# Optimization experiments

Measured on AMD Instinct MI355X. Metric: run time of the kernel, lower is better.

Reference implementation:

```python
import jax, jax.numpy as jnp
import numpy as np

NUM_CENTROID = 64
HIDDEN = 768
MAX_SEQ = 128
D = MAX_SEQ * HIDDEN  # 98304 flattened feature dim
NUM_ITERS = 10        # fixed Lloyd iterations (original loops to tol; fixed for jit)


def _cdist(x, c):
    x2 = jnp.sum(x * x, axis=-1, keepdims=True)          # [N,1]
    c2 = jnp.sum(c * c, axis=-1)                          # [K]
    d2 = x2 + c2[None, :] - 2.0 * (x @ c.T)               # [N,K]
    return jnp.sqrt(jnp.maximum(d2, 0.0))


def setup_inputs() -> dict:
    key = jax.random.key(0)
    k1, k2 = jax.random.split(key)
    x = jax.random.normal(k1, (1024, MAX_SEQ, HIDDEN), dtype=jnp.float32)
    # centroid table initialized as Normal(mean=0.07, std=0.39) per the module
    centroid = 0.07 + 0.39 * jax.random.normal(k2, (NUM_CENTROID, D), dtype=jnp.float32)
    return {"x": x, "centroid": centroid}


def reference(x, centroid):
    X = x.reshape(-1, D)                                  # [N, D]
    N = X.shape[0]
    # 'resuming' branch: snap each centroid to its nearest sample
    dis0 = _cdist(X, centroid)                            # [N, K]
    choice_points = jnp.argmin(dis0, axis=0)              # [K]
    state = X[choice_points]                              # [K, D]
    ones = jnp.ones((N,), dtype=X.dtype)

    def step(state, _):
        dis = _cdist(X, state)                            # [N, K]
        choice = jnp.argmin(dis, axis=1)                  # [N]
        sums = jax.ops.segment_sum(X, choice, num_segments=NUM_CENTROID)   # [K, D]
        counts = jax.ops.segment_sum(ones, choice, num_segments=NUM_CENTROID)  # [K]
        nonempty = counts[:, None] > 0
        new_state = jnp.where(nonempty, sums / jnp.maximum(counts[:, None], 1.0), state)
        return new_state, choice

    state, choices = jax.lax.scan(step, state, None, length=NUM_ITERS)
    # returns (new centroids, final cluster assignments) like the module
    return state, choices[-1]
```

## Files before the change

### kernel.cpp

```cpp
#include <hip/hip_runtime.h>
#include <cstddef>
#include <cstdint>


#define N_PTS  1024
#define K_C    64
#define D_DIM  98304
#define ITERS  10
#define SPLITD 64
#define BM     64
#define DC     64
#define LDSP   72
#define NCHK   96
#define CCHK   12

typedef __attribute__((ext_vector_type(8))) short bf16x8;
typedef __attribute__((ext_vector_type(8))) unsigned short ushort8;
typedef __attribute__((ext_vector_type(4))) float f32x4;

__device__ __forceinline__ unsigned short f2bf(float x) {
    unsigned u = __float_as_uint(x);
    u = (u + 0x7FFFu + ((u >> 16) & 1u)) >> 16;
    return (unsigned short)u;
}
__device__ __forceinline__ float bf2f(unsigned short b) {
    return __uint_as_float((unsigned)b << 16);
}
__device__ __forceinline__ void cvt2(float x, unsigned short& h, unsigned short& l) {
    h = f2bf(x);
    l = f2bf(x - bf2f(h));
}

__device__ __forceinline__ float block_sum256(float s) {
    #pragma unroll
    for (int o = 32; o; o >>= 1) s += __shfl_down(s, o);
    __shared__ float red[4];
    int lane = threadIdx.x & 63, w = threadIdx.x >> 6;
    if (lane == 0) red[w] = s;
    __syncthreads();
    return red[0] + red[1] + red[2] + red[3];
}

__global__ __launch_bounds__(256) void convert_kernel(const float* __restrict__ A,
                                                      unsigned short* __restrict__ Ph,
                                                      unsigned short* __restrict__ Pl,
                                                      float* __restrict__ sq_part) {
    const int n = blockIdx.x, j = blockIdx.y;
    const size_t base = (size_t)n * D_DIM + (size_t)j * 8192;
    const int t = threadIdx.x;
    float ss = 0.f;
    #pragma unroll
    for (int i = 0; i < 4; ++i) {
        size_t e = base + (size_t)i * 2048 + t * 8;
        float4 a = *reinterpret_cast<const float4*>(A + e);
        float4 b = *reinterpret_cast<const float4*>(A + e + 4);
        ss += a.x*a.x + a.y*a.y + a.z*a.z + a.w*a.w;
        ss += b.x*b.x + b.y*b.y + b.z*b.z + b.w*b.w;
        ushort4 h0, l0, h1, l1;
        cvt2(a.x, h0.x, l0.x); cvt2(a.y, h0.y, l0.y);
        cvt2(a.z, h0.z, l0.z); cvt2(a.w, h0.w, l0.w);
        cvt2(b.x, h1.x, l1.x); cvt2(b.y, h1.y, l1.y);
        cvt2(b.z, h1.z, l1.z); cvt2(b.w, h1.w, l1.w);
        *reinterpret_cast<ushort4*>(Ph + e)     = h0;
        *reinterpret_cast<ushort4*>(Ph + e + 4) = h1;
        *reinterpret_cast<ushort4*>(Pl + e)     = l0;
        *reinterpret_cast<ushort4*>(Pl + e + 4) = l1;
    }
    ss = block_sum256(ss);
    if (t == 0) sq_part[n * CCHK + j] = ss;
}

__global__ __launch_bounds__(256) void reduce_sq_kernel(const float* __restrict__ sq_part,
                                                        float* __restrict__ out, int rows) {
    int n = blockIdx.x * 256 + threadIdx.x;
    if (n >= rows) return;
    float s = 0.f;
    #pragma unroll
    for (int j = 0; j < CCHK; ++j) s += sq_part[n * CCHK + j];
    out[n] = s;
}

__global__ __launch_bounds__(256, 5) void mfma_dot_kernel(const unsigned short* __restrict__ Xh,
                                                          const unsigned short* __restrict__ Xl,
                                                          const unsigned short* __restrict__ Sh,
                                                          const unsigned short* __restrict__ Sl,
                                                          float* __restrict__ partial) {
    __shared__ alignas(16) short Bh[K_C][LDSP];
    __shared__ alignas(16) short Bl[K_C][LDSP];

    const int seg = blockIdx.x, nblk = blockIdx.y;
    const int t = threadIdx.x;
    const int wid = t >> 6, lane = t & 63;
    const int d_begin = seg * (D_DIM / SPLITD);
    const int NCH = (D_DIM / SPLITD) / DC;

    const int arow = nblk * BM + wid * 16 + (lane & 15);
    const int ko = (lane >> 4) * 8;
    const unsigned short* xh = Xh + (size_t)arow * D_DIM;
    const unsigned short* xl = Xl + (size_t)arow * D_DIM;

    const int sr = t >> 2, sc = (t & 3) * 16;
    const unsigned short* shp = Sh + (size_t)sr * D_DIM;
    const unsigned short* slp = Sl + (size_t)sr * D_DIM;

    ushort8 s0, s1, s2, s3;
    bf16x8 aEh0, aEh1, aEl0, aEl1;
    bf16x8 aOh0, aOh1, aOl0, aOl1;

    auto loadB = [&](int d0) {
        s0 = *reinterpret_cast<const ushort8*>(shp + d0 + sc);
        s1 = *reinterpret_cast<const ushort8*>(shp + d0 + sc + 8);
        s2 = *reinterpret_cast<const ushort8*>(slp + d0 + sc);
        s3 = *reinterpret_cast<const ushort8*>(slp + d0 + sc + 8);
    };
    auto storeB = [&]() {
        *reinterpret_cast<ushort8*>(&Bh[sr][sc])     = s0;
        *reinterpret_cast<ushort8*>(&Bh[sr][sc + 8]) = s1;
        *reinterpret_cast<ushort8*>(&Bl[sr][sc])     = s2;
        *reinterpret_cast<ushort8*>(&Bl[sr][sc + 8]) = s3;
    };

    f32x4 acc[4];
    #pragma unroll
    for (int i = 0; i < 4; ++i) acc[i] = f32x4{0.f, 0.f, 0.f, 0.f};

    #define LOADA(bh0, bh1, bl0, bl1, d0)                                        \
        bh0 = *reinterpret_cast<const bf16x8*>(xh + (d0) + ko);                  \
        bh1 = *reinterpret_cast<const bf16x8*>(xh + (d0) + 32 + ko);             \
        bl0 = *reinterpret_cast<const bf16x8*>(xl + (d0) + ko);                  \
        bl1 = *reinterpret_cast<const bf16x8*>(xl + (d0) + 32 + ko);

    #define MFMAS(ah0, ah1, al0, al1)                                            \
        _Pragma("unroll")                                                        \
        for (int nb = 0; nb < 4; ++nb) {                                         \
            const int br = nb * 16 + (lane & 15);                                \
            bf16x8 bh = *reinterpret_cast<const bf16x8*>(&Bh[br][ko]);           \
            bf16x8 bl = *reinterpret_cast<const bf16x8*>(&Bl[br][ko]);           \
            acc[nb] = __builtin_amdgcn_mfma_f32_16x16x32_bf16(ah0, bh, acc[nb], 0, 0, 0); \
            acc[nb] = __builtin_amdgcn_mfma_f32_16x16x32_bf16(ah0, bl, acc[nb], 0, 0, 0); \
            acc[nb] = __builtin_amdgcn_mfma_f32_16x16x32_bf16(al0, bh, acc[nb], 0, 0, 0); \
        }                                                                        \
        _Pragma("unroll")                                                        \
        for (int nb = 0; nb < 4; ++nb) {                                         \
            const int br = nb * 16 + (lane & 15);                                \
            bf16x8 bh = *reinterpret_cast<const bf16x8*>(&Bh[br][32 + ko]);      \
            bf16x8 bl = *reinterpret_cast<const bf16x8*>(&Bl[br][32 + ko]);      \
            acc[nb] = __builtin_amdgcn_mfma_f32_16x16x32_bf16(ah1, bh, acc[nb], 0, 0, 0); \
            acc[nb] = __builtin_amdgcn_mfma_f32_16x16x32_bf16(ah1, bl, acc[nb], 0, 0, 0); \
            acc[nb] = __builtin_amdgcn_mfma_f32_16x16x32_bf16(al1, bh, acc[nb], 0, 0, 0); \
        }

    loadB(d_begin);
    LOADA(aEh0, aEh1, aEl0, aEl1, d_begin);
    for (int c = 0; c < NCH; c += 2) {
        __syncthreads();
        storeB();
        __syncthreads();
        {
            int dn = d_begin + (c + 1) * DC;
            loadB(dn);
            LOADA(aOh0, aOh1, aOl0, aOl1, dn);
        }
        MFMAS(aEh0, aEh1, aEl0, aEl1);
        __syncthreads();
        storeB();
        __syncthreads();
        if (c + 2 < NCH) {
            int dn = d_begin + (c + 2) * DC;
            loadB(dn);
            LOADA(aEh0, aEh1, aEl0, aEl1, dn);
        }
        MFMAS(aOh0, aOh1, aOl0, aOl1);
    }
    #undef LOADA
    #undef MFMAS

    #pragma unroll
    for (int nb = 0; nb < 4; ++nb)
        #pragma unroll
        for (int r = 0; r < 4; ++r) {
            int row = wid * 16 + (lane >> 4) * 4 + r;
            int col = nb * 16 + (lane & 15);
            int n = nblk * BM + row;
            partial[((size_t)seg * N_PTS + n) * K_C + col] = acc[nb][r];
        }
}

__global__ __launch_bounds__(256) void reduce_dot_kernel(const float* __restrict__ partial,
                                                         float* __restrict__ dot) {
    int i = blockIdx.x * 256 + threadIdx.x;
    float s = 0.f;
    #pragma unroll 8
    for (int p = 0; p < SPLITD; ++p) s += partial[(size_t)p * N_PTS * K_C + i];
    dot[i] = s;
}

__global__ __launch_bounds__(256) void argmin_n_kernel(const float* __restrict__ dot,
                                                       const float* __restrict__ x2,
                                                       int* __restrict__ choice_pts) {
    int k = blockIdx.x;
    float best = 3.4e38f; int bi = N_PTS;
    for (int n = threadIdx.x; n < N_PTS; n += 256) {
        float v = fmaf(-2.f, dot[n * K_C + k], x2[n]);
        if (v < best || (v == best && n < bi)) { best = v; bi = n; }
    }
    #pragma unroll
    for (int off = 32; off; off >>= 1) {
        float v2 = __shfl_down(best, off);
        int   i2 = __shfl_down(bi, off);
        if (v2 < best || (v2 == best && i2 < bi)) { best = v2; bi = i2; }
    }
    __shared__ float bv[4]; __shared__ int bix[4];
    int lane = threadIdx.x & 63, wid = threadIdx.x >> 6;
    if (lane == 0) { bv[wid] = best; bix[wid] = bi; }
    __syncthreads();
    if (threadIdx.x == 0) {
        for (int w = 1; w < 4; ++w)
            if (bv[w] < best || (bv[w] == best && bix[w] < bi)) { best = bv[w]; bi = bix[w]; }
        choice_pts[k] = bi;
    }
}

__global__ __launch_bounds__(256) void gather_kernel(const float* __restrict__ X,
                                                     const int* __restrict__ choice_pts,
                                                     float* __restrict__ state,
                                                     unsigned short* __restrict__ Sh,
                                                     unsigned short* __restrict__ Sl,
                                                     float* __restrict__ c2p) {
    int k = blockIdx.x;
    int c = choice_pts[k];
    size_t d = (size_t)blockIdx.y * 1024 + threadIdx.x * 4;
    size_t o = (size_t)k * D_DIM + d;
    float4 v = *reinterpret_cast<const float4*>(X + (size_t)c * D_DIM + d);
    *reinterpret_cast<float4*>(state + o) = v;
    ushort4 h, l;
    cvt2(v.x, h.x, l.x); cvt2(v.y, h.y, l.y); cvt2(v.z, h.z, l.z); cvt2(v.w, h.w, l.w);
    *reinterpret_cast<ushort4*>(Sh + o) = h;
    *reinterpret_cast<ushort4*>(Sl + o) = l;
    float ss = block_sum256(v.x*v.x + v.y*v.y + v.z*v.z + v.w*v.w);
    if (threadIdx.x == 0) c2p[k * NCHK + blockIdx.y] = ss;
}

__global__ __launch_bounds__(256) void assign_kernel(const float* __restrict__ partial,
                                                     const float* __restrict__ c2p,
                                                     int* __restrict__ choice) {
    int wid = threadIdx.x >> 6, lane = threadIdx.x & 63;
    int n = blockIdx.x * 4 + wid;
    float s = 0.f;
    #pragma unroll 8
    for (int p = 0; p < SPLITD; ++p) s += partial[((size_t)p * N_PTS + n) * K_C + lane];
    float c2 = 0.f;
    const float* cp2 = c2p + lane * NCHK;
    #pragma unroll 8
    for (int j = 0; j < NCHK; ++j) c2 += cp2[j];
    float v = fmaf(-2.f, s, c2);
    int bi = lane;
    #pragma unroll
    for (int m = 32; m; m >>= 1) {
        float v2 = __shfl_xor(v, m);
        int   i2 = __shfl_xor(bi, m);
        if (v2 < v || (v2 == v && i2 < bi)) { v = v2; bi = i2; }
    }
    if (lane == 0) choice[n] = bi;
}

__global__ __launch_bounds__(256) void init_prev_kernel(int* __restrict__ chp,
                                                        int* __restrict__ ctp) {
    int t = blockIdx.x * 256 + threadIdx.x;
    if (t < N_PTS) chp[t] = -1;
    if (t < K_C)   ctp[t] = 0;
}

__global__ __launch_bounds__(1024) void changes_kernel(const int* __restrict__ ch_new,
                                                       const int* __restrict__ ch_prev,
                                                       int* __restrict__ add_n,
                                                       int* __restrict__ astart,
                                                       int* __restrict__ sub_n,
                                                       int* __restrict__ sstart,
                                                       int* __restrict__ counts_new) {
    __shared__ int chn[N_PTS];
    __shared__ int chp[N_PTS];
    __shared__ int acnt[K_C], scnt[K_C], hcnt[K_C];
    __shared__ int ast[K_C + 1], sst[K_C + 1];
    const int t = threadIdx.x;
    if (t < K_C) { acnt[t] = 0; scnt[t] = 0; hcnt[t] = 0; }
    __syncthreads();
    const int cn = ch_new[t], cp = ch_prev[t];
    chn[t] = cn; chp[t] = cp;
    atomicAdd(&hcnt[cn], 1);
    const bool changed = (cn != cp);
    if (changed) {
        atomicAdd(&acnt[cn], 1);
        if (cp >= 0) atomicAdd(&scnt[cp], 1);
    }
    __syncthreads();
    if (t == 0) {
        int a = 0;
        for (int k = 0; k < K_C; ++k) { ast[k] = a; a += acnt[k]; }
        ast[K_C] = a;
    }
    if (t == 64) {
        int a = 0;
        for (int k = 0; k < K_C; ++k) { sst[k] = a; a += scnt[k]; }
        sst[K_C] = a;
    }
    __syncthreads();
    int ra = 0, rs = 0;
    for (int m = 0; m < t; ++m) {
        int cm = chn[m], pm = chp[m];
        bool ch = (cm != pm);
        ra += (ch && cm == cn);
        rs += (ch && pm == cp);
    }
    if (changed) {
        add_n[ast[cn] + ra] = t;
        if (cp >= 0) sub_n[sst[cp] + rs] = t;
    }
    if (t <= K_C) { astart[t] = ast[t]; sstart[t] = sst[t]; }
    if (t < K_C) counts_new[t] = hcnt[t];
}

__global__ __launch_bounds__(256) void update_kernel(const float* __restrict__ X,
                                                     const int* __restrict__ add_n,
                                                     const int* __restrict__ astart,
                                                     const int* __restrict__ sub_n,
                                                     const int* __restrict__ sstart,
                                                     const int* __restrict__ counts_new,
                                                     const int* __restrict__ counts_prev,
                                                     float* __restrict__ state,
                                                     unsigned short* __restrict__ Sh,
                                                     unsigned short* __restrict__ Sl,
                                                     float* __restrict__ c2p) {
    const int k = blockIdx.x;
    const int ab = astart[k], ae = astart[k + 1];
    const int sb = sstart[k], se = sstart[k + 1];
    if (ab == ae && sb == se) return;
    const int cn = counts_new[k], cp = counts_prev[k];
    const size_t d = (size_t)blockIdx.y * 1024 + threadIdx.x * 4;
    const size_t o = (size_t)k * D_DIM + d;

    float sx = 0.f, sy = 0.f, sz = 0.f, sw = 0.f;
    if (cp > 0) {
        float4 st = *reinterpret_cast<const float4*>(state + o);
        float c = (float)cp;
        sx = st.x * c; sy = st.y * c; sz = st.z * c; sw = st.w * c;
    }
    for (int i = ab; i < ae; ++i) {
        const float4 v = *reinterpret_cast<const float4*>(X + (size_t)add_n[i] * D_DIM + d);
        sx += v.x; sy += v.y; sz += v.z; sw += v.w;
    }
    for (int i = sb; i < se; ++i) {
        const float4 v = *reinterpret_cast<const float4*>(X + (size_t)sub_n[i] * D_DIM + d);
        sx -= v.x; sy -= v.y; sz -= v.z; sw -= v.w;
    }
    if (cn > 0) {
        float inv = 1.f / (float)cn;
        float4 m; m.x = sx * inv; m.y = sy * inv; m.z = sz * inv; m.w = sw * inv;
        *reinterpret_cast<float4*>(state + o) = m;
        ushort4 h, l;
        cvt2(m.x, h.x, l.x); cvt2(m.y, h.y, l.y); cvt2(m.z, h.z, l.z); cvt2(m.w, h.w, l.w);
        *reinterpret_cast<ushort4*>(Sh + o) = h;
        *reinterpret_cast<ushort4*>(Sl + o) = l;
        float ss = block_sum256(m.x*m.x + m.y*m.y + m.z*m.z + m.w*m.w);
        if (threadIdx.x == 0) c2p[k * NCHK + blockIdx.y] = ss;
    }
}

__global__ __launch_bounds__(256) void choice_out_kernel(const int* __restrict__ choice,
                                                         float* __restrict__ out) {
    int n = blockIdx.x * 256 + threadIdx.x;
    if (n < N_PTS) out[n] = (float)choice[n];
}

extern "C" void kernel_launch(void* const* d_in, const int* in_sizes, int n_in,
                              void* d_out, int out_size, void* d_ws, size_t ws_size,
                              hipStream_t stream) {
    const float* X  = (const float*)d_in[0];
    const float* C0 = (const float*)d_in[1];
    float* state      = (float*)d_out;
    float* out_choice = state + (size_t)K_C * D_DIM;

    char* w = (char*)d_ws;
    size_t off = 0;
    auto alloc = [&](size_t bytes) { void* p = w + off; off = (off + bytes + 255) & ~(size_t)255; return p; };
    unsigned short* Xh = (unsigned short*)alloc((size_t)N_PTS * D_DIM * 2);
    unsigned short* Xl = (unsigned short*)alloc((size_t)N_PTS * D_DIM * 2);
    unsigned short* Sh = (unsigned short*)alloc((size_t)K_C * D_DIM * 2);
    unsigned short* Sl = (unsigned short*)alloc((size_t)K_C * D_DIM * 2);
    float* partial = (float*)alloc((size_t)SPLITD * N_PTS * K_C * 4);
    float* dotb    = (float*)alloc((size_t)N_PTS * K_C * 4);
    float* x2p     = (float*)alloc((size_t)N_PTS * CCHK * 4);
    float* x2      = (float*)alloc((size_t)N_PTS * 4);
    float* c0sq    = (float*)alloc((size_t)K_C * CCHK * 4);
    float* c2p     = (float*)alloc((size_t)K_C * NCHK * 4);
    int* cpts      = (int*)alloc(256);
    int* ch[2];
    ch[0] = (int*)alloc((size_t)N_PTS * 4);
    ch[1] = (int*)alloc((size_t)N_PTS * 4);
    int* ct[2];
    ct[0] = (int*)alloc(256);
    ct[1] = (int*)alloc(256);
    int* add_n  = (int*)alloc((size_t)N_PTS * 4);
    int* astart = (int*)alloc(512);
    int* sub_n  = (int*)alloc((size_t)N_PTS * 4);
    int* sstart = (int*)alloc(512);

    dim3 b256(256);

    convert_kernel<<<dim3(N_PTS, CCHK), b256, 0, stream>>>(X, Xh, Xl, x2p);
    reduce_sq_kernel<<<dim3(4), b256, 0, stream>>>(x2p, x2, N_PTS);

    convert_kernel<<<dim3(K_C, CCHK), b256, 0, stream>>>(C0, Sh, Sl, c0sq);
    mfma_dot_kernel<<<dim3(SPLITD, N_PTS / BM), b256, 0, stream>>>(Xh, Xl, Sh, Sl, partial);
    reduce_dot_kernel<<<dim3(N_PTS * K_C / 256), b256, 0, stream>>>(partial, dotb);
    argmin_n_kernel<<<K_C, b256, 0, stream>>>(dotb, x2, cpts);
    gather_kernel<<<dim3(K_C, NCHK), b256, 0, stream>>>(X, cpts, state, Sh, Sl, c2p);
    init_prev_kernel<<<dim3(4), b256, 0, stream>>>(ch[0], ct[0]);

    for (int it = 0; it < ITERS; ++it) {
        int prev = it & 1, cur = 1 - prev;
        mfma_dot_kernel<<<dim3(SPLITD, N_PTS / BM), b256, 0, stream>>>(Xh, Xl, Sh, Sl, partial);
        assign_kernel<<<dim3(N_PTS / 4), b256, 0, stream>>>(partial, c2p, ch[cur]);
        changes_kernel<<<1, dim3(1024), 0, stream>>>(ch[cur], ch[prev], add_n, astart,
                                                     sub_n, sstart, ct[cur]);
        update_kernel<<<dim3(K_C, NCHK), b256, 0, stream>>>(X, add_n, astart, sub_n, sstart,
                                                            ct[cur], ct[prev], state, Sh, Sl, c2p);
    }

    choice_out_kernel<<<dim3(N_PTS / 256), b256, 0, stream>>>(ch[0], out_choice);
}
```

Baseline: 2.011 ms.

## Run Lloyd iterations in Gram-matrix space instead of recomputing full-D distances

Builds the 1024x1024 Gram matrix X·Xᵀ once with split-bf16 MFMA, then expresses every centroid dot product and centroid norm as averages of Gram entries over cluster members. Each iteration touches only the Gram matrix and small index arrays rather than the 98304-wide data. The centroid table is materialised from X only once at the end, using the last iteration in which each cluster was non-empty. This adds a large Gram build and a workspace buffer, and it changes floating-point summation order, which could flip near-tie assignments.

Result: slower. 2.179 ms (+8.4%).

```diff
diff --git a/kernel.cpp b/kernel.cpp
--- a/kernel.cpp
+++ b/kernel.cpp
@@ -13,6 +13,11 @@
 #define LDSP   72
 #define NCHK   96
 #define CCHK   12
+#define GSEG   16
+#define NPAIR  36
+#define GT     128
+#define GDC    32
+#define GLP    40
 
 typedef __attribute__((ext_vector_type(8))) short bf16x8;
 typedef __attribute__((ext_vector_type(8))) unsigned short ushort8;
@@ -223,37 +228,152 @@
 
 __global__ __launch_bounds__(256) void gather_kernel(const float* __restrict__ X,
                                                      const int* __restrict__ choice_pts,
-                                                     float* __restrict__ state,
-                                                     unsigned short* __restrict__ Sh,
-                                                     unsigned short* __restrict__ Sl,
-                                                     float* __restrict__ c2p) {
+                                                     float* __restrict__ state) {
     int k = blockIdx.x;
     int c = choice_pts[k];
     size_t d = (size_t)blockIdx.y * 1024 + threadIdx.x * 4;
-    size_t o = (size_t)k * D_DIM + d;
     float4 v = *reinterpret_cast<const float4*>(X + (size_t)c * D_DIM + d);
-    *reinterpret_cast<float4*>(state + o) = v;
-    ushort4 h, l;
-    cvt2(v.x, h.x, l.x); cvt2(v.y, h.y, l.y); cvt2(v.z, h.z, l.z); cvt2(v.w, h.w, l.w);
-    *reinterpret_cast<ushort4*>(Sh + o) = h;
-    *reinterpret_cast<ushort4*>(Sl + o) = l;
-    float ss = block_sum256(v.x*v.x + v.y*v.y + v.z*v.z + v.w*v.w);
-    if (threadIdx.x == 0) c2p[k * NCHK + blockIdx.y] = ss;
-}
-
-__global__ __launch_bounds__(256) void assign_kernel(const float* __restrict__ partial,
-                                                     const float* __restrict__ c2p,
-                                                     int* __restrict__ choice) {
+    *reinterpret_cast<float4*>(state + (size_t)k * D_DIM + d) = v;
+}
+
+__global__ __launch_bounds__(256) void gbuild_kernel(const unsigned short* __restrict__ Xh,
+                                                     const unsigned short* __restrict__ Xl,
+                                                     float* __restrict__ Gpart) {
+    __shared__ alignas(16) short Ah[GT][GLP];
+    __shared__ alignas(16) short Al[GT][GLP];
+    __shared__ alignas(16) short Bh[GT][GLP];
+    __shared__ alignas(16) short Bl[GT][GLP];
+
+    const int p = blockIdx.x, seg = blockIdx.y;
+    int bi = 0, rem = p, rl = 8;
+    while (rem >= rl) { rem -= rl; --rl; ++bi; }
+    const int bj = bi + rem;
+
+    const int t = threadIdx.x;
+    const int wid = t >> 6, lane = t & 63;
+    const int wr = wid >> 1, wc = wid & 1;
+    const int d_begin = seg * (D_DIM / GSEG);
+    const int NCH = (D_DIM / GSEG) / GDC;
+
+    const int srow = t >> 1;
+    const int scol = (t & 1) << 4;
+    const unsigned short* gah = Xh + (size_t)(bi * GT + srow) * D_DIM;
+    const unsigned short* gal = Xl + (size_t)(bi * GT + srow) * D_DIM;
+    const unsigned short* gbh = Xh + (size_t)(bj * GT + srow) * D_DIM;
+    const unsigned short* gbl = Xl + (size_t)(bj * GT + srow) * D_DIM;
+
+    ushort8 ra0, ra1, ra2, ra3, rb0, rb1, rb2, rb3;
+    auto loadRegs = [&](int d0) {
+        ra0 = *reinterpret_cast<const ushort8*>(gah + d0 + scol);
+        ra1 = *reinterpret_cast<const ushort8*>(gah + d0 + scol + 8);
+        ra2 = *reinterpret_cast<const ushort8*>(gal + d0 + scol);
+        ra3 = *reinterpret_cast<const ushort8*>(gal + d0 + scol + 8);
+        rb0 = *reinterpret_cast<const ushort8*>(gbh + d0 + scol);
+        rb1 = *reinterpret_cast<const ushort8*>(gbh + d0 + scol + 8);
+        rb2 = *reinterpret_cast<const ushort8*>(gbl + d0 + scol);
+        rb3 = *reinterpret_cast<const ushort8*>(gbl + d0 + scol + 8);
+    };
+    auto storeRegs = [&]() {
+        *reinterpret_cast<ushort8*>(&Ah[srow][scol])     = ra0;
+        *reinterpret_cast<ushort8*>(&Ah[srow][scol + 8]) = ra1;
+        *reinterpret_cast<ushort8*>(&Al[srow][scol])     = ra2;
+        *reinterpret_cast<ushort8*>(&Al[srow][scol + 8]) = ra3;
+        *reinterpret_cast<ushort8*>(&Bh[srow][scol])     = rb0;
+        *reinterpret_cast<ushort8*>(&Bh[srow][scol + 8]) = rb1;
+        *reinterpret_cast<ushort8*>(&Bl[srow][scol])     = rb2;
+        *reinterpret_cast<ushort8*>(&Bl[srow][scol + 8]) = rb3;
+    };
+
+    f32x4 acc[4][4];
+    #pragma unroll
+    for (int i = 0; i < 4; ++i)
+        #pragma unroll
+        for (int j = 0; j < 4; ++j) acc[i][j] = f32x4{0.f, 0.f, 0.f, 0.f};
+
+    const int rbase = wr * 64 + (lane & 15);
+    const int cbase = wc * 64 + (lane & 15);
+    const int ko = (lane >> 4) * 8;
+
+    loadRegs(d_begin);
+    for (int c = 0; c < NCH; ++c) {
+        __syncthreads();
+        storeRegs();
+        __syncthreads();
+        if (c + 1 < NCH) loadRegs(d_begin + (c + 1) * GDC);
+        bf16x8 fah[4], fal[4], fbh[4], fbl[4];
+        #pragma unroll
+        for (int f = 0; f < 4; ++f) {
+            fah[f] = *reinterpret_cast<const bf16x8*>(&Ah[rbase + f * 16][ko]);
+            fal[f] = *reinterpret_cast<const bf16x8*>(&Al[rbase + f * 16][ko]);
+            fbh[f] = *reinterpret_cast<const bf16x8*>(&Bh[cbase + f * 16][ko]);
+            fbl[f] = *reinterpret_cast<const bf16x8*>(&Bl[cbase + f * 16][ko]);
+        }
+        #pragma unroll
+        for (int fi = 0; fi < 4; ++fi)
+            #pragma unroll
+            for (int fj = 0; fj < 4; ++fj) {
+                acc[fi][fj] = __builtin_amdgcn_mfma_f32_16x16x32_bf16(fah[fi], fbh[fj], acc[fi][fj], 0, 0, 0);
+                acc[fi][fj] = __builtin_amdgcn_mfma_f32_16x16x32_bf16(fah[fi], fbl[fj], acc[fi][fj], 0, 0, 0);
+                acc[fi][fj] = __builtin_amdgcn_mfma_f32_16x16x32_bf16(fal[fi], fbh[fj], acc[fi][fj], 0, 0, 0);
+            }
+    }
+
+    float* gp = Gpart + ((size_t)seg * NPAIR + p) * (GT * GT);
+    #pragma unroll
+    for (int fi = 0; fi < 4; ++fi)
+        #pragma unroll
+        for (int fj = 0; fj < 4; ++fj)
+            #pragma unroll
+            for (int r = 0; r < 4; ++r) {
+                int row = wr * 64 + fi * 16 + (lane >> 4) * 4 + r;
+                int col = wc * 64 + fj * 16 + (lane & 15);
+                gp[row * GT + col] = acc[fi][fj][r];
+            }
+}
+
+__global__ __launch_bounds__(256) void reduce_g_kernel(const float* __restrict__ Gpart,
+                                                       float* __restrict__ G) {
+    const int p = blockIdx.x, blk = blockIdx.y;
+    int bi = 0, rem = p, rl = 8;
+    while (rem >= rl) { rem -= rl; --rl; ++bi; }
+    const int bj = bi + rem;
+    const int e0 = blk * 1024 + threadIdx.x * 4;
+    float sx = 0.f, sy = 0.f, sz = 0.f, sw = 0.f;
+    #pragma unroll
+    for (int g = 0; g < GSEG; ++g) {
+        const float4 v = *reinterpret_cast<const float4*>(
+            Gpart + ((size_t)g * NPAIR + p) * (GT * GT) + e0);
+        sx += v.x; sy += v.y; sz += v.z; sw += v.w;
+    }
+    const int row = e0 >> 7, col = e0 & 127;
+    const int gi = bi * GT + row, gj = bj * GT + col;
+    float4 o = {sx, sy, sz, sw};
+    *reinterpret_cast<float4*>(&G[(size_t)gi * N_PTS + gj]) = o;
+    if (bi != bj) {
+        G[(size_t)(gj + 0) * N_PTS + gi] = sx;
+        G[(size_t)(gj + 1) * N_PTS + gi] = sy;
+        G[(size_t)(gj + 2) * N_PTS + gi] = sz;
+        G[(size_t)(gj + 3) * N_PTS + gi] = sw;
+    }
+}
+
+__global__ __launch_bounds__(256) void dot0_kernel(const float* __restrict__ G,
+                                                   const int* __restrict__ cpts,
+                                                   const float* __restrict__ x2,
+                                                   float* __restrict__ dot,
+                                                   float* __restrict__ c2) {
+    int g = blockIdx.x * 256 + threadIdx.x;
+    int n = g >> 6, k = g & 63;
+    dot[g] = G[(size_t)n * N_PTS + cpts[k]];
+    if (g < K_C) c2[g] = x2[cpts[g]];
+}
+
+__global__ __launch_bounds__(256) void assign_g_kernel(const float* __restrict__ dot,
+                                                       const float* __restrict__ c2,
+                                                       int* __restrict__ choice_it) {
     int wid = threadIdx.x >> 6, lane = threadIdx.x & 63;
     int n = blockIdx.x * 4 + wid;
-    float s = 0.f;
-    #pragma unroll 8
-    for (int p = 0; p < SPLITD; ++p) s += partial[((size_t)p * N_PTS + n) * K_C + lane];
-    float c2 = 0.f;
-    const float* cp2 = c2p + lane * NCHK;
-    #pragma unroll 8
-    for (int j = 0; j < NCHK; ++j) c2 += cp2[j];
-    float v = fmaf(-2.f, s, c2);
+    float v = fmaf(-2.f, dot[n * K_C + lane], c2[lane]);
     int bi = lane;
     #pragma unroll
     for (int m = 32; m; m >>= 1) {
@@ -261,109 +381,100 @@
         int   i2 = __shfl_xor(bi, m);
         if (v2 < v || (v2 == v && i2 < bi)) { v = v2; bi = i2; }
     }
-    if (lane == 0) choice[n] = bi;
-}
-
-__global__ __launch_bounds__(256) void init_prev_kernel(int* __restrict__ chp,
-                                                        int* __restrict__ ctp) {
-    int t = blockIdx.x * 256 + threadIdx.x;
-    if (t < N_PTS) chp[t] = -1;
-    if (t < K_C)   ctp[t] = 0;
-}
-
-__global__ __launch_bounds__(1024) void changes_kernel(const int* __restrict__ ch_new,
-                                                       const int* __restrict__ ch_prev,
-                                                       int* __restrict__ add_n,
-                                                       int* __restrict__ astart,
-                                                       int* __restrict__ sub_n,
-                                                       int* __restrict__ sstart,
-                                                       int* __restrict__ counts_new) {
-    __shared__ int chn[N_PTS];
-    __shared__ int chp[N_PTS];
-    __shared__ int acnt[K_C], scnt[K_C], hcnt[K_C];
-    __shared__ int ast[K_C + 1], sst[K_C + 1];
-    const int t = threadIdx.x;
-    if (t < K_C) { acnt[t] = 0; scnt[t] = 0; hcnt[t] = 0; }
-    __syncthreads();
-    const int cn = ch_new[t], cp = ch_prev[t];
-    chn[t] = cn; chp[t] = cp;
-    atomicAdd(&hcnt[cn], 1);
-    const bool changed = (cn != cp);
-    if (changed) {
-        atomicAdd(&acnt[cn], 1);
-        if (cp >= 0) atomicAdd(&scnt[cp], 1);
-    }
+    if (lane == 0) choice_it[n] = bi;
+}
+
+__global__ __launch_bounds__(1024) void sort2_kernel(const int* __restrict__ choice,
+                                                     int* __restrict__ order,
+                                                     int* __restrict__ cstart,
+                                                     int* __restrict__ tlast,
+                                                     int it) {
+    __shared__ int ch[N_PTS];
+    __shared__ int cnt[K_C];
+    __shared__ int cst[K_C + 1];
+    int t = threadIdx.x;
+    if (t < K_C) cnt[t] = 0;
+    __syncthreads();
+    int c = choice[t];
+    ch[t] = c;
+    atomicAdd(&cnt[c], 1);
     __syncthreads();
     if (t == 0) {
         int a = 0;
-        for (int k = 0; k < K_C; ++k) { ast[k] = a; a += acnt[k]; }
-        ast[K_C] = a;
-    }
-    if (t == 64) {
-        int a = 0;
-        for (int k = 0; k < K_C; ++k) { sst[k] = a; a += scnt[k]; }
-        sst[K_C] = a;
-    }
-    __syncthreads();
-    int ra = 0, rs = 0;
-    for (int m = 0; m < t; ++m) {
-        int cm = chn[m], pm = chp[m];
-        bool ch = (cm != pm);
-        ra += (ch && cm == cn);
-        rs += (ch && pm == cp);
-    }
-    if (changed) {
-        add_n[ast[cn] + ra] = t;
-        if (cp >= 0) sub_n[sst[cp] + rs] = t;
-    }
-    if (t <= K_C) { astart[t] = ast[t]; sstart[t] = sst[t]; }
-    if (t < K_C) counts_new[t] = hcnt[t];
-}
-
-__global__ __launch_bounds__(256) void update_kernel(const float* __restrict__ X,
-                                                     const int* __restrict__ add_n,
-                                                     const int* __restrict__ astart,
-                                                     const int* __restrict__ sub_n,
-                                                     const int* __restrict__ sstart,
-                                                     const int* __restrict__ counts_new,
-                                                     const int* __restrict__ counts_prev,
-                                                     float* __restrict__ state,
-                                                     unsigned short* __restrict__ Sh,
-                                                     unsigned short* __restrict__ Sl,
-                                                     float* __restrict__ c2p) {
+        for (int k = 0; k < K_C; ++k) { cst[k] = a; a += cnt[k]; }
+        cst[K_C] = a;
+    }
+    __syncthreads();
+    if (t <= K_C) cstart[t] = cst[t];
+    if (t < K_C && cnt[t] > 0) tlast[t] = it;
+    int r = 0;
+    for (int m = 0; m < t; ++m) r += (ch[m] == c);
+    order[cst[c] + r] = t;
+}
+
+__global__ __launch_bounds__(256) void dotup_kernel(const float* __restrict__ G,
+                                                    const int* __restrict__ order,
+                                                    const int* __restrict__ cstart,
+                                                    float* __restrict__ dot) {
+    __shared__ int ord[N_PTS];
+    __shared__ int cst[K_C + 1];
+    int t = threadIdx.x;
+    #pragma unroll
+    for (int i = 0; i < 4; ++i) ord[t + 256 * i] = order[t + 256 * i];
+    if (t <= K_C) cst[t] = cstart[t];
+    __syncthreads();
+    int wid = t >> 6, lane = t & 63;
+    int n = blockIdx.x * 4 + wid;
+    int b = cst[lane], e = cst[lane + 1];
+    if (b == e) return;
+    const float* gr = G + (size_t)n * N_PTS;
+    float s = 0.f;
+    for (int i = b; i < e; ++i) s += gr[ord[i]];
+    dot[n * K_C + lane] = s / (float)(e - b);
+}
+
+__global__ __launch_bounds__(64) void c2up_kernel(const float* __restrict__ dot,
+                                                  const int* __restrict__ order,
+                                                  const int* __restrict__ cstart,
+                                                  float* __restrict__ c2) {
+    int k = threadIdx.x;
+    int b = cstart[k], e = cstart[k + 1];
+    if (b == e) return;
+    float s = 0.f;
+    for (int i = b; i < e; ++i) s += dot[order[i] * K_C + k];
+    c2[k] = s / (float)(e - b);
+}
+
+__global__ __launch_bounds__(64) void init_tlast_kernel(int* __restrict__ tlast) {
+    tlast[threadIdx.x] = -1;
+}
+
+__global__ __launch_bounds__(256) void final_state_kernel(const float* __restrict__ X,
+                                                          const int* __restrict__ chbuf,
+                                                          const int* __restrict__ tlast,
+                                                          float* __restrict__ state) {
     const int k = blockIdx.x;
-    const int ab = astart[k], ae = astart[k + 1];
-    const int sb = sstart[k], se = sstart[k + 1];
-    if (ab == ae && sb == se) return;
-    const int cn = counts_new[k], cp = counts_prev[k];
-    const size_t d = (size_t)blockIdx.y * 1024 + threadIdx.x * 4;
-    const size_t o = (size_t)k * D_DIM + d;
-
+    const int tk = tlast[k];
+    if (tk < 0) return;
+    __shared__ int chs[N_PTS];
+    const int* src = chbuf + tk * N_PTS;
+    const int t = threadIdx.x;
+    #pragma unroll
+    for (int i = 0; i < 4; ++i) chs[t + 256 * i] = src[t + 256 * i];
+    __syncthreads();
+    const size_t d = (size_t)blockIdx.y * 1024 + t * 4;
     float sx = 0.f, sy = 0.f, sz = 0.f, sw = 0.f;
-    if (cp > 0) {
-        float4 st = *reinterpret_cast<const float4*>(state + o);
-        float c = (float)cp;
-        sx = st.x * c; sy = st.y * c; sz = st.z * c; sw = st.w * c;
-    }
-    for (int i = ab; i < ae; ++i) {
-        const float4 v = *reinterpret_cast<const float4*>(X + (size_t)add_n[i] * D_DIM + d);
-        sx += v.x; sy += v.y; sz += v.z; sw += v.w;
-    }
-    for (int i = sb; i < se; ++i) {
-        const float4 v = *reinterpret_cast<const float4*>(X + (size_t)sub_n[i] * D_DIM + d);
-        sx -= v.x; sy -= v.y; sz -= v.z; sw -= v.w;
-    }
-    if (cn > 0) {
-        float inv = 1.f / (float)cn;
-        float4 m; m.x = sx * inv; m.y = sy * inv; m.z = sz * inv; m.w = sw * inv;
-        *reinterpret_cast<float4*>(state + o) = m;
-        ushort4 h, l;
-        cvt2(m.x, h.x, l.x); cvt2(m.y, h.y, l.y); cvt2(m.z, h.z, l.z); cvt2(m.w, h.w, l.w);
-        *reinterpret_cast<ushort4*>(Sh + o) = h;
-        *reinterpret_cast<ushort4*>(Sl + o) = l;
-        float ss = block_sum256(m.x*m.x + m.y*m.y + m.z*m.z + m.w*m.w);
-        if (threadIdx.x == 0) c2p[k * NCHK + blockIdx.y] = ss;
-    }
+    int cm = 0;
+    for (int n = 0; n < N_PTS; ++n) {
+        if (chs[n] == k) {
+            ++cm;
+            const float4 v = *reinterpret_cast<const float4*>(X + (size_t)n * D_DIM + d);
+            sx += v.x; sy += v.y; sz += v.z; sw += v.w;
+        }
+    }
+    float inv = 1.f / (float)cm;
+    float4 o = {sx * inv, sy * inv, sz * inv, sw * inv};
+    *reinterpret_cast<float4*>(state + (size_t)k * D_DIM + d) = o;
 }
 
 __global__ __launch_bounds__(256) void choice_out_kernel(const int* __restrict__ choice,
@@ -388,44 +499,45 @@
     unsigned short* Sh = (unsigned short*)alloc((size_t)K_C * D_DIM * 2);
     unsigned short* Sl = (unsigned short*)alloc((size_t)K_C * D_DIM * 2);
     float* partial = (float*)alloc((size_t)SPLITD * N_PTS * K_C * 4);
+    float* Gpart   = (float*)alloc((size_t)GSEG * NPAIR * GT * GT * 4);
+    float* G       = (float*)alloc((size_t)N_PTS * N_PTS * 4);
     float* dotb    = (float*)alloc((size_t)N_PTS * K_C * 4);
     float* x2p     = (float*)alloc((size_t)N_PTS * CCHK * 4);
     float* x2      = (float*)alloc((size_t)N_PTS * 4);
     float* c0sq    = (float*)alloc((size_t)K_C * CCHK * 4);
-    float* c2p     = (float*)alloc((size_t)K_C * NCHK * 4);
+    float* dotg    = (float*)alloc((size_t)N_PTS * K_C * 4);
+    float* c2      = (float*)alloc(256);
     int* cpts      = (int*)alloc(256);
-    int* ch[2];
-    ch[0] = (int*)alloc((size_t)N_PTS * 4);
-    ch[1] = (int*)alloc((size_t)N_PTS * 4);
-    int* ct[2];
-    ct[0] = (int*)alloc(256);
-    ct[1] = (int*)alloc(256);
-    int* add_n  = (int*)alloc((size_t)N_PTS * 4);
-    int* astart = (int*)alloc(512);
-    int* sub_n  = (int*)alloc((size_t)N_PTS * 4);
-    int* sstart = (int*)alloc(512);
+    int* chbuf     = (int*)alloc((size_t)ITERS * N_PTS * 4);
+    int* order     = (int*)alloc((size_t)N_PTS * 4);
+    int* cstart    = (int*)alloc(512);
+    int* tlast     = (int*)alloc(256);
 
     dim3 b256(256);
 
     convert_kernel<<<dim3(N_PTS, CCHK), b256, 0, stream>>>(X, Xh, Xl, x2p);
     reduce_sq_kernel<<<dim3(4), b256, 0, stream>>>(x2p, x2, N_PTS);
+
+    gbuild_kernel<<<dim3(NPAIR, GSEG), b256, 0, stream>>>(Xh, Xl, Gpart);
+    reduce_g_kernel<<<dim3(NPAIR, 16), b256, 0, stream>>>(Gpart, G);
 
     convert_kernel<<<dim3(K_C, CCHK), b256, 0, stream>>>(C0, Sh, Sl, c0sq);
     mfma_dot_kernel<<<dim3(SPLITD, N_PTS / BM), b256, 0, stream>>>(Xh, Xl, Sh, Sl, partial);
     reduce_dot_kernel<<<dim3(N_PTS * K_C / 256), b256, 0, stream>>>(partial, dotb);
     argmin_n_kernel<<<K_C, b256, 0, stream>>>(dotb, x2, cpts);
-    gather_kernel<<<dim3(K_C, NCHK), b256, 0, stream>>>(X, cpts, state, Sh, Sl, c2p);
-    init_prev_kernel<<<dim3(4), b256, 0, stream>>>(ch[0], ct[0]);
+    gather_kernel<<<dim3(K_C, NCHK), b256, 0, stream>>>(X, cpts, state);
+    init_tlast_kernel<<<1, dim3(64), 0, stream>>>(tlast);
+    dot0_kernel<<<dim3(N_PTS * K_C / 256), b256, 0, stream>>>(G, cpts, x2, dotg, c2);
 
     for (int it = 0; it < ITERS; ++it) {
-        int prev = it & 1, cur = 1 - prev;
-        mfma_dot_kernel<<<dim3(SPLITD, N_PTS / BM), b256, 0, stream>>>(Xh, Xl, Sh, Sl, partial);
-        assign_kernel<<<dim3(N_PTS / 4), b256, 0, stream>>>(partial, c2p, ch[cur]);
-        changes_kernel<<<1, dim3(1024), 0, stream>>>(ch[cur], ch[prev], add_n, astart,
-                                                     sub_n, sstart, ct[cur]);
-        update_kernel<<<dim3(K_C, NCHK), b256, 0, stream>>>(X, add_n, astart, sub_n, sstart,
-                                                            ct[cur], ct[prev], state, Sh, Sl, c2p);
-    }
-
-    choice_out_kernel<<<dim3(N_PTS / 256), b256, 0, stream>>>(ch[0], out_choice);
-}
+        assign_g_kernel<<<dim3(N_PTS / 4), b256, 0, stream>>>(dotg, c2, chbuf + it * N_PTS);
+        sort2_kernel<<<1, dim3(1024), 0, stream>>>(chbuf + it * N_PTS, order, cstart, tlast, it);
+        if (it < ITERS - 1) {
+            dotup_kernel<<<dim3(N_PTS / 4), b256, 0, stream>>>(G, order, cstart, dotg);
+            c2up_kernel<<<1, dim3(64), 0, stream>>>(dotg, order, cstart, c2);
+        }
+    }
+
+    final_state_kernel<<<dim3(K_C, NCHK), b256, 0, stream>>>(X, chbuf, tlast, state);
+    choice_out_kernel<<<dim3(N_PTS / 256), b256, 0, stream>>>(chbuf + (ITERS - 1) * N_PTS, out_choice);
+}
```
